# Kernel tuning notes

Hardware: AMD Instinct MI355X
Metric: run time of the kernel (lower is better)

## Reference

```python
import jax, jax.numpy as jnp
import numpy as np

H = 32  # hidden_size


def gru_layer(x, W_ih, W_hh, b_ih, b_hh):
    """PyTorch-semantics single-layer GRU, batch_first. x: [B,T,I] -> [B,T,H]."""
    # Precompute input projections for all timesteps (one big GEMM).
    gi = jnp.einsum('bti,gi->btg', x, W_ih) + b_ih  # [B,T,3H], gate order r,z,n

    def step(h, gi_t):
        gh = h @ W_hh.T + b_hh                      # [B,3H]
        i_r, i_z, i_n = jnp.split(gi_t, 3, axis=-1)
        h_r, h_z, h_n = jnp.split(gh, 3, axis=-1)
        r = jax.nn.sigmoid(i_r + h_r)
        z = jax.nn.sigmoid(i_z + h_z)
        n = jnp.tanh(i_n + r * h_n)
        h_new = (1.0 - z) * n + z * h
        return h_new, h_new

    h0 = jnp.zeros((x.shape[0], W_hh.shape[1]), x.dtype)
    _, ys = jax.lax.scan(step, h0, jnp.swapaxes(gi, 0, 1))  # scan over T
    return jnp.swapaxes(ys, 0, 1)                            # [B,T,H]


def setup_inputs() -> dict:
    key = jax.random.key(0)
    ks = jax.random.split(key, 13)
    N, C, T = 64, 8, 1024
    s = 0.1
    inp = {"x": jax.random.normal(ks[0], (N, C, T), dtype=jnp.float32)}
    # layer 1: input_size=1; layers 2,3: input_size=H
    inp["W_ih1"] = jax.random.normal(ks[1], (3 * H, 1), dtype=jnp.float32) * s
    inp["W_hh1"] = jax.random.normal(ks[2], (3 * H, H), dtype=jnp.float32) * s
    inp["b_ih1"] = jax.random.normal(ks[3], (3 * H,), dtype=jnp.float32) * s
    inp["b_hh1"] = jax.random.normal(ks[4], (3 * H,), dtype=jnp.float32) * s
    inp["W_ih2"] = jax.random.normal(ks[5], (3 * H, H), dtype=jnp.float32) * s
    inp["W_hh2"] = jax.random.normal(ks[6], (3 * H, H), dtype=jnp.float32) * s
    inp["b_ih2"] = jax.random.normal(ks[7], (3 * H,), dtype=jnp.float32) * s
    inp["b_hh2"] = jax.random.normal(ks[8], (3 * H,), dtype=jnp.float32) * s
    inp["W_ih3"] = jax.random.normal(ks[9], (3 * H, H), dtype=jnp.float32) * s
    inp["W_hh3"] = jax.random.normal(ks[10], (3 * H, H), dtype=jnp.float32) * s
    inp["b_ih3"] = jax.random.normal(ks[11], (3 * H,), dtype=jnp.float32) * s
    inp["b_hh3"] = jax.random.normal(ks[12], (3 * H,), dtype=jnp.float32) * s
    return inp


def reference(x, W_ih1, W_hh1, b_ih1, b_hh1,
              W_ih2, W_hh2, b_ih2, b_hh2,
              W_ih3, W_hh3, b_ih3, b_hh3):
    N, C, T = x.shape
    y = x.reshape(N * C, T, 1)                 # [N*C, T, 1]
    y = gru_layer(y, W_ih1, W_hh1, b_ih1, b_hh1)
    y = gru_layer(y, W_ih2, W_hh2, b_ih2, b_hh2)
    y = gru_layer(y, W_ih3, W_hh3, b_ih3, b_hh3)  # [N*C, T, H]
    # Faithful to original (including its permute-then-view layout scramble):
    out = jnp.transpose(y, (1, 0, 2)).reshape(N, C, T, H)
    return out
```

## Files before the change

### kernel.cpp

```cpp
#include <hip/hip_runtime.h>

#define TT 1024

typedef float v2f __attribute__((ext_vector_type(2)));

__device__ __forceinline__ v2f pk_mul(v2f a, v2f b) {
    v2f d; asm("v_pk_mul_f32 %0, %1, %2" : "=v"(d) : "v"(a), "v"(b)); return d;
}
__device__ __forceinline__ v2f pk_fma(v2f a, v2f b, v2f c) {
    v2f d; asm("v_pk_fma_f32 %0, %1, %2, %3" : "=v"(d) : "v"(a), "v"(b), "v"(c)); return d;
}
__device__ __forceinline__ v2f pk_add(v2f a, v2f b) {
    v2f d; asm("v_pk_add_f32 %0, %1, %2" : "=v"(d) : "v"(a), "v"(b)); return d;
}

__device__ __forceinline__ float fast_sigmoid(float x) {
    float e = __builtin_amdgcn_exp2f(x * -1.4426950408889634f);
    return __builtin_amdgcn_rcpf(1.0f + e);
}
__device__ __forceinline__ float fast_tanh(float x) {
    float e = __builtin_amdgcn_exp2f(x * -2.8853900817779268f);
    return fmaf(2.0f, __builtin_amdgcn_rcpf(1.0f + e), -1.0f);
}

__device__ __forceinline__ void dot3(const v2f (&w)[3][8], const v2f (&v)[8], float (&d)[3]) {
#pragma unroll
    for (int g = 0; g < 3; ++g) {
        v2f a = pk_mul(w[g][0], v[0]);
        v2f b = pk_mul(w[g][1], v[1]);
        a = pk_fma(w[g][2], v[2], a);
        b = pk_fma(w[g][3], v[3], b);
        a = pk_fma(w[g][4], v[4], a);
        b = pk_fma(w[g][5], v[5], b);
        a = pk_fma(w[g][6], v[6], a);
        b = pk_fma(w[g][7], v[7], b);
        a = pk_add(a, b);
        d[g] = a.x + a.y;
    }
}

__device__ __forceinline__ void load8(const float* p, v2f (&v)[8]) {
    const float4 f0 = ((const float4*)p)[0];
    const float4 f1 = ((const float4*)p)[1];
    const float4 f2 = ((const float4*)p)[2];
    const float4 f3 = ((const float4*)p)[3];
    v[0] = v2f{f0.x, f0.y}; v[1] = v2f{f0.z, f0.w};
    v[2] = v2f{f1.x, f1.y}; v[3] = v2f{f1.z, f1.w};
    v[4] = v2f{f2.x, f2.y}; v[5] = v2f{f2.z, f2.w};
    v[6] = v2f{f3.x, f3.y}; v[7] = v2f{f3.z, f3.w};
}

__device__ __forceinline__ void sync_lgkm() {
    __builtin_amdgcn_sched_barrier(0);
    asm volatile("s_waitcnt lgkmcnt(0)" ::: "memory");
    __builtin_amdgcn_s_barrier();
    __builtin_amdgcn_sched_barrier(0);
}

__global__ __launch_bounds__(192, 2) void gru3_fused(
    const float* __restrict__ x,
    const float* __restrict__ Wih1, const float* __restrict__ Whh1,
    const float* __restrict__ bih1, const float* __restrict__ bhh1,
    const float* __restrict__ Wih2, const float* __restrict__ Whh2,
    const float* __restrict__ bih2, const float* __restrict__ bhh2,
    const float* __restrict__ Wih3, const float* __restrict__ Whh3,
    const float* __restrict__ bih3, const float* __restrict__ bhh3,
    float* __restrict__ out)
{
    __shared__ float ybuf[3 * 2 * 32];
    __shared__ float xs[TT];

    const int tid  = threadIdx.x;
    const int wid  = __builtin_amdgcn_readfirstlane(tid >> 6);
    const int lane = tid & 63;
    const int h    = lane & 31;
    const int kh   = lane >> 5;
    const int k0   = kh * 16;
    const int bb   = (int)blockIdx.x;

    if (tid < 192) ybuf[tid] = 0.0f;
    {
        const float4* xr4 = (const float4*)(x + bb * TT);
        for (int j = tid; j < TT / 4; j += 192) ((float4*)xs)[j] = xr4[j];
    }

    const float* WhhP = (wid == 0) ? Whh1 : (wid == 1) ? Whh2 : Whh3;
    const float* WihP = (wid == 0) ? Whh1 : (wid == 1) ? Wih2 : Wih3;
    v2f whh[3][8], wih[3][8];
#pragma unroll
    for (int g = 0; g < 3; ++g) {
        load8(WhhP + (g * 32 + h) * 32 + k0, whh[g]);
        load8(WihP + (g * 32 + h) * 32 + k0, wih[g]);
    }
    if (wid != 0) {
#pragma unroll
        for (int g = 0; g < 3; ++g)
#pragma unroll
            for (int j = 0; j < 8; ++j) {
                asm volatile("" : "+v"(whh[g][j]));
                asm volatile("" : "+v"(wih[g][j]));
            }
    } else {
#pragma unroll
        for (int g = 0; g < 3; ++g)
#pragma unroll
            for (int j = 0; j < 8; ++j)
                asm volatile("" : "+v"(whh[g][j]));
    }

    const float* bihp = (wid == 0) ? bih1 : (wid == 1) ? bih2 : bih3;
    const float* bhhp = (wid == 0) ? bhh1 : (wid == 1) ? bhh2 : bhh3;
    const float brz_r = bihp[h]      + bhhp[h];
    const float brz_z = bihp[32 + h] + bhhp[32 + h];
    const float b_in  = bihp[64 + h];
    const float b_hn  = bhhp[64 + h];
    float wi_r = 0.f, wi_z = 0.f, wi_n = 0.f;
    if (wid == 0) { wi_r = Wih1[h]; wi_z = Wih1[32 + h]; wi_n = Wih1[64 + h]; }

    __syncthreads();

    float hprev = 0.0f;
    for (int i = 0; i < TT + 2; ++i) {
        const int t = i - wid;
        if (t >= 0 && t < TT) {
            const int p = t & 1;

            v2f vi[8], vo[8];
            if (wid != 0) load8(ybuf + (wid - 1) * 64 + p * 32 + k0, vi);
            load8(ybuf + wid * 64 + (p ^ 1) * 32 + k0, vo);

            float di[3], dh[3];
            float xv = 0.f;
            if (wid == 0) xv = xs[t];
            if (wid != 0) dot3(wih, vi, di);
            dot3(whh, vo, dh);

            float r, z, nn;
            if (wid != 0) {
                float cr = dh[0] + di[0]; cr += __shfl_xor(cr, 32);
                float cz = dh[1] + di[1]; cz += __shfl_xor(cz, 32);
                float ci = di[2];         ci += __shfl_xor(ci, 32);
                float ch = dh[2];         ch += __shfl_xor(ch, 32);
                r  = fast_sigmoid(cr + brz_r);
                z  = fast_sigmoid(cz + brz_z);
                nn = fast_tanh(ci + b_in + r * (ch + b_hn));
            } else {
                float sr = dh[0]; sr += __shfl_xor(sr, 32);
                float sz = dh[1]; sz += __shfl_xor(sz, 32);
                float sn = dh[2]; sn += __shfl_xor(sn, 32);
                r  = fast_sigmoid(fmaf(xv, wi_r, sr + brz_r));
                z  = fast_sigmoid(fmaf(xv, wi_z, sz + brz_z));
                nn = fast_tanh(fmaf(xv, wi_n, b_in) + r * (sn + b_hn));
            }
            const float hn = fmaf(z, hprev - nn, nn);
            hprev = hn;

            if (kh == 0) {
                ybuf[wid * 64 + p * 32 + h] = hn;
                if (wid == 2) out[t * 16384 + bb * 32 + h] = hn;
            }
        }
        sync_lgkm();
    }
}

extern "C" void kernel_launch(void* const* d_in, const int* in_sizes, int n_in,
                              void* d_out, int out_size, void* d_ws, size_t ws_size,
                              hipStream_t stream) {
    const float* x    = (const float*)d_in[0];
    const float* Wih1 = (const float*)d_in[1];
    const float* Whh1 = (const float*)d_in[2];
    const float* bih1 = (const float*)d_in[3];
    const float* bhh1 = (const float*)d_in[4];
    const float* Wih2 = (const float*)d_in[5];
    const float* Whh2 = (const float*)d_in[6];
    const float* bih2 = (const float*)d_in[7];
    const float* bhh2 = (const float*)d_in[8];
    const float* Wih3 = (const float*)d_in[9];
    const float* Whh3 = (const float*)d_in[10];
    const float* bih3 = (const float*)d_in[11];
    const float* bhh3 = (const float*)d_in[12];

    gru3_fused<<<dim3(512), dim3(192), 0, stream>>>(
        x, Wih1, Whh1, bih1, bhh1,
        Wih2, Whh2, bih2, bhh2,
        Wih3, Whh3, bih3, bhh3,
        (float*)d_out);
}
```

Measured before the change: 644.3 us.

## Process two sequences per block to interleave independent recurrences

Each block now runs two batch sequences through the fused three-layer GRU pipeline, doubling the LDS ping-pong buffers and the staged input. Each wave computes both sequences' dot products and gates and stores one per half-wave, with the grid halved. The aim is to amortize the per-timestep barrier and LDS latency over twice the work and expose instruction-level parallelism. The cost is more VALU work per step and higher register pressure, with fewer blocks per CU available to hide latency.

```diff
diff --git a/kernel.cpp b/kernel.cpp
--- a/kernel.cpp
+++ b/kernel.cpp
@@ -57,6 +57,8 @@
     __builtin_amdgcn_sched_barrier(0);
 }
 
+#define YB(L, p, s) ((((L) * 2 + (p)) * 2 + (s)) * 32)
+
 __global__ __launch_bounds__(192, 2) void gru3_fused(
     const float* __restrict__ x,
     const float* __restrict__ Wih1, const float* __restrict__ Whh1,
@@ -67,8 +69,8 @@
     const float* __restrict__ bih3, const float* __restrict__ bhh3,
     float* __restrict__ out)
 {
-    __shared__ float ybuf[3 * 2 * 32];
-    __shared__ float xs[TT];
+    __shared__ float ybuf[3 * 2 * 2 * 32];
+    __shared__ float xs[2 * TT];
 
     const int tid  = threadIdx.x;
     const int wid  = __builtin_amdgcn_readfirstlane(tid >> 6);
@@ -78,10 +80,10 @@
     const int k0   = kh * 16;
     const int bb   = (int)blockIdx.x;
 
-    if (tid < 192) ybuf[tid] = 0.0f;
+    if (tid < 192) { ybuf[tid] = 0.0f; ybuf[192 + tid] = 0.0f; }
     {
-        const float4* xr4 = (const float4*)(x + bb * TT);
-        for (int j = tid; j < TT / 4; j += 192) ((float4*)xs)[j] = xr4[j];
+        const float4* xr4 = (const float4*)(x + 2 * bb * TT);
+        for (int j = tid; j < 2 * TT / 4; j += 192) ((float4*)xs)[j] = xr4[j];
     }
 
     const float* WhhP = (wid == 0) ? Whh1 : (wid == 1) ? Whh2 : Whh3;
@@ -92,21 +94,13 @@
         load8(WhhP + (g * 32 + h) * 32 + k0, whh[g]);
         load8(WihP + (g * 32 + h) * 32 + k0, wih[g]);
     }
-    if (wid != 0) {
-#pragma unroll
-        for (int g = 0; g < 3; ++g)
-#pragma unroll
-            for (int j = 0; j < 8; ++j) {
-                asm volatile("" : "+v"(whh[g][j]));
-                asm volatile("" : "+v"(wih[g][j]));
-            }
-    } else {
-#pragma unroll
-        for (int g = 0; g < 3; ++g)
-#pragma unroll
-            for (int j = 0; j < 8; ++j)
-                asm volatile("" : "+v"(whh[g][j]));
-    }
+#pragma unroll
+    for (int g = 0; g < 3; ++g)
+#pragma unroll
+        for (int j = 0; j < 8; ++j) {
+            asm volatile("" : "+v"(whh[g][j]));
+            asm volatile("" : "+v"(wih[g][j]));
+        }
 
     const float* bihp = (wid == 0) ? bih1 : (wid == 1) ? bih2 : bih3;
     const float* bhhp = (wid == 0) ? bhh1 : (wid == 1) ? bhh2 : bhh3;
@@ -119,46 +113,71 @@
 
     __syncthreads();
 
-    float hprev = 0.0f;
+    float hp0 = 0.0f, hp1 = 0.0f;
     for (int i = 0; i < TT + 2; ++i) {
         const int t = i - wid;
         if (t >= 0 && t < TT) {
             const int p = t & 1;
 
-            v2f vi[8], vo[8];
-            if (wid != 0) load8(ybuf + (wid - 1) * 64 + p * 32 + k0, vi);
-            load8(ybuf + wid * 64 + (p ^ 1) * 32 + k0, vo);
-
-            float di[3], dh[3];
-            float xv = 0.f;
-            if (wid == 0) xv = xs[t];
-            if (wid != 0) dot3(wih, vi, di);
-            dot3(whh, vo, dh);
-
-            float r, z, nn;
+            float r0, z0, n0, r1, z1, n1;
             if (wid != 0) {
-                float cr = dh[0] + di[0]; cr += __shfl_xor(cr, 32);
-                float cz = dh[1] + di[1]; cz += __shfl_xor(cz, 32);
-                float ci = di[2];         ci += __shfl_xor(ci, 32);
-                float ch = dh[2];         ch += __shfl_xor(ch, 32);
-                r  = fast_sigmoid(cr + brz_r);
-                z  = fast_sigmoid(cz + brz_z);
-                nn = fast_tanh(ci + b_in + r * (ch + b_hn));
+                v2f vi0[8], vi1[8], vo0[8], vo1[8];
+                load8(ybuf + YB(wid - 1, p, 0) + k0, vi0);
+                load8(ybuf + YB(wid - 1, p, 1) + k0, vi1);
+                load8(ybuf + YB(wid, p ^ 1, 0) + k0, vo0);
+                load8(ybuf + YB(wid, p ^ 1, 1) + k0, vo1);
+
+                float di0[3], dh0[3], di1[3], dh1[3];
+                dot3(wih, vi0, di0);
+                dot3(wih, vi1, di1);
+                dot3(whh, vo0, dh0);
+                dot3(whh, vo1, dh1);
+
+                float cr0 = dh0[0] + di0[0]; cr0 += __shfl_xor(cr0, 32);
+                float cz0 = dh0[1] + di0[1]; cz0 += __shfl_xor(cz0, 32);
+                float ci0 = di0[2];          ci0 += __shfl_xor(ci0, 32);
+                float ch0 = dh0[2];          ch0 += __shfl_xor(ch0, 32);
+                float cr1 = dh1[0] + di1[0]; cr1 += __shfl_xor(cr1, 32);
+                float cz1 = dh1[1] + di1[1]; cz1 += __shfl_xor(cz1, 32);
+                float ci1 = di1[2];          ci1 += __shfl_xor(ci1, 32);
+                float ch1 = dh1[2];          ch1 += __shfl_xor(ch1, 32);
+
+                r0 = fast_sigmoid(cr0 + brz_r);
+                z0 = fast_sigmoid(cz0 + brz_z);
+                n0 = fast_tanh(ci0 + b_in + r0 * (ch0 + b_hn));
+                r1 = fast_sigmoid(cr1 + brz_r);
+                z1 = fast_sigmoid(cz1 + brz_z);
+                n1 = fast_tanh(ci1 + b_in + r1 * (ch1 + b_hn));
             } else {
-                float sr = dh[0]; sr += __shfl_xor(sr, 32);
-                float sz = dh[1]; sz += __shfl_xor(sz, 32);
-                float sn = dh[2]; sn += __shfl_xor(sn, 32);
-                r  = fast_sigmoid(fmaf(xv, wi_r, sr + brz_r));
-                z  = fast_sigmoid(fmaf(xv, wi_z, sz + brz_z));
-                nn = fast_tanh(fmaf(xv, wi_n, b_in) + r * (sn + b_hn));
+                const float xv0 = xs[t];
+                const float xv1 = xs[TT + t];
+                v2f vo0[8], vo1[8];
+                load8(ybuf + YB(0, p ^ 1, 0) + k0, vo0);
+                load8(ybuf + YB(0, p ^ 1, 1) + k0, vo1);
+                float dh0[3], dh1[3];
+                dot3(whh, vo0, dh0);
+                dot3(whh, vo1, dh1);
+                float sr0 = dh0[0]; sr0 += __shfl_xor(sr0, 32);
+                float sz0 = dh0[1]; sz0 += __shfl_xor(sz0, 32);
+                float sn0 = dh0[2]; sn0 += __shfl_xor(sn0, 32);
+                float sr1 = dh1[0]; sr1 += __shfl_xor(sr1, 32);
+                float sz1 = dh1[1]; sz1 += __shfl_xor(sz1, 32);
+                float sn1 = dh1[2]; sn1 += __shfl_xor(sn1, 32);
+                r0 = fast_sigmoid(fmaf(xv0, wi_r, sr0 + brz_r));
+                z0 = fast_sigmoid(fmaf(xv0, wi_z, sz0 + brz_z));
+                n0 = fast_tanh(fmaf(xv0, wi_n, b_in) + r0 * (sn0 + b_hn));
+                r1 = fast_sigmoid(fmaf(xv1, wi_r, sr1 + brz_r));
+                z1 = fast_sigmoid(fmaf(xv1, wi_z, sz1 + brz_z));
+                n1 = fast_tanh(fmaf(xv1, wi_n, b_in) + r1 * (sn1 + b_hn));
             }
-            const float hn = fmaf(z, hprev - nn, nn);
-            hprev = hn;
-
-            if (kh == 0) {
-                ybuf[wid * 64 + p * 32 + h] = hn;
-                if (wid == 2) out[t * 16384 + bb * 32 + h] = hn;
-            }
+            const float hn0 = fmaf(z0, hp0 - n0, n0);
+            const float hn1 = fmaf(z1, hp1 - n1, n1);
+            hp0 = hn0; hp1 = hn1;
+
+            const float hsel = kh ? hn1 : hn0;
+            ybuf[YB(wid, p, kh) + h] = hsel;
+            if (wid == 2)
+                out[t * 16384 + (2 * bb + kh) * 32 + h] = hsel;
         }
         sync_lgkm();
     }
@@ -181,7 +200,7 @@
     const float* bih3 = (const float*)d_in[11];
     const float* bhh3 = (const float*)d_in[12];
 
-    gru3_fused<<<dim3(512), dim3(192), 0, stream>>>(
+    gru3_fused<<<dim3(256), dim3(192), 0, stream>>>(
         x, Wih1, Whh1, bih1, bhh1,
         Wih2, Whh2, bih2, bhh2,
         Wih3, Whh3, bih3, bhh3,
```

Measured after the change: 871.7 us. +35.3%, slower.
